# Kernel optimization log

Hardware: AMD Instinct MI355X
Metric: run time of the kernel (lower is better)

Reference implementation:

```python
import jax, jax.numpy as jnp
import numpy as np

B, T, H = 4, 2048, 512
HEADS = 8
D = H // HEADS  # head dim = 64


def setup_inputs() -> dict:
    key = jax.random.key(0)
    ks = jax.random.split(key, 5)
    s = 1.0 / np.sqrt(H)
    return {
        "x": jax.random.normal(ks[0], (B, T, H), dtype=jnp.float32),
        "w_qkv": jax.random.uniform(ks[1], (H, 3 * H), dtype=jnp.float32, minval=-s, maxval=s),
        "b_qkv": jax.random.uniform(ks[2], (3 * H,), dtype=jnp.float32, minval=-s, maxval=s),
        "w_proj": jax.random.uniform(ks[3], (H, H), dtype=jnp.float32, minval=-s, maxval=s),
        "b_proj": jax.random.uniform(ks[4], (H,), dtype=jnp.float32, minval=-s, maxval=s),
    }


def reference(x, w_qkv, b_qkv, w_proj, b_proj):
    b, t, h = x.shape
    scale = (h // HEADS) ** (-0.5)
    qkv = (x @ w_qkv + b_qkv).reshape(b, t, 3, HEADS, h // HEADS)
    q, k, v = qkv[:, :, 0], qkv[:, :, 1], qkv[:, :, 2]  # [b,t,heads,d]
    q = q * scale
    scores = jnp.einsum('bthd,bThd->bhtT', q, k)  # [b,heads,t,t]
    weights = jax.nn.softmax(scores, axis=-1)
    attn = jnp.einsum('bhtT,bThd->bthd', weights, v).reshape(b, t, h)
    return attn @ w_proj + b_proj
```

## Files before the change

kernel.cpp:

```cpp
#include <hip/hip_runtime.h>
#include <stdint.h>

typedef unsigned short u16;
typedef __attribute__((ext_vector_type(8))) __bf16 bf16x8;
typedef __attribute__((ext_vector_type(4))) __bf16 bf16x4;
typedef __attribute__((ext_vector_type(4))) float f32x4;
typedef __attribute__((ext_vector_type(2))) unsigned int u32x2;
typedef __attribute__((ext_vector_type(4))) unsigned int u32x4;

#define QSCALE 0.18033688011112042f

__device__ __forceinline__ u16 f2bf(float f) {
    uint32_t u = __builtin_bit_cast(uint32_t, f);
    u = (u + 0x7fffu + ((u >> 16) & 1u)) >> 16;
    return (u16)u;
}
__device__ __forceinline__ float bf2f(u16 h) {
    uint32_t u = ((uint32_t)h) << 16;
    return __builtin_bit_cast(float, u);
}

__device__ __forceinline__ void gl_lds16(const u16* g, u16* l) {
    __builtin_amdgcn_global_load_lds(
        (__attribute__((address_space(1))) uint32_t*)(g),
        (__attribute__((address_space(3))) uint32_t*)(l), 16, 0, 0);
}

__global__ __launch_bounds__(256) void convert_x_k(const float* __restrict__ xf,
                                                   u16* __restrict__ xbf) {
    const size_t v = (size_t)blockIdx.x * 256 + threadIdx.x;
    const f32x4 val = ((const f32x4*)xf)[v];
    u32x2 p;
    p.x = (uint32_t)f2bf(val.x) | ((uint32_t)f2bf(val.y) << 16);
    p.y = (uint32_t)f2bf(val.z) | ((uint32_t)f2bf(val.w) << 16);
    *(u32x2*)&xbf[v * 4] = p;
}

__global__ void transpose_cvt_k(const float* __restrict__ in,
                                u16* __restrict__ out, int R, int C) {
    __shared__ u16 t[64][65];
    const int bx = blockIdx.x << 6, by = blockIdx.y << 6;
    const int tx = threadIdx.x, ty = threadIdx.y;
#pragma unroll
    for (int i = ty; i < 64; i += 8)
        t[i][tx] = f2bf(in[(size_t)(by + i) * C + bx + tx]);
    __syncthreads();
#pragma unroll
    for (int i = ty; i < 64; i += 8) out[(size_t)(bx + i) * R + by + tx] = t[tx][i];
}

template <int EPI>
__global__ __launch_bounds__(256) void gemm_bt_k(
    const u16* __restrict__ A, const u16* __restrict__ Bt,
    const float* __restrict__ bias,
    u16* __restrict__ Qb, u16* __restrict__ Kb, u16* __restrict__ Vt,
    float* __restrict__ OutF) {
    __shared__ u16 lA[128 * 32];
    __shared__ u16 lB[128 * 32];
    const int tid = threadIdx.x;
    const int w = tid >> 6, l = tid & 63, quad = l >> 4, r = l & 15;
    const int tm = blockIdx.x << 7, tn = blockIdx.y << 7;
    const int wm = (w >> 1) << 6, wn = (w & 1) << 6;
    const int srow = l >> 2, sch = (l & 3) << 3;

    f32x4 acc[4][4];
#pragma unroll
    for (int i = 0; i < 4; ++i)
#pragma unroll
        for (int j = 0; j < 4; ++j) acc[i][j] = (f32x4){0.f, 0.f, 0.f, 0.f};

    for (int kk = 0; kk < 512; kk += 32) {
        __syncthreads();
#pragma unroll
        for (int ii = 0; ii < 2; ++ii) {
            const int rowl = w * 32 + ii * 16;
            gl_lds16(A + (size_t)(tm + rowl + srow) * 512 + kk + sch, &lA[rowl * 32]);
            gl_lds16(Bt + (size_t)(tn + rowl + srow) * 512 + kk + sch, &lB[rowl * 32]);
        }
        __syncthreads();
        bf16x8 af[4], bfr[4];
#pragma unroll
        for (int mi = 0; mi < 4; ++mi)
            af[mi] = *(const bf16x8*)&lA[(wm + mi * 16 + r) * 32 + quad * 8];
#pragma unroll
        for (int ni = 0; ni < 4; ++ni)
            bfr[ni] = *(const bf16x8*)&lB[(wn + ni * 16 + r) * 32 + quad * 8];
#pragma unroll
        for (int mi = 0; mi < 4; ++mi)
#pragma unroll
            for (int ni = 0; ni < 4; ++ni)
                acc[mi][ni] = __builtin_amdgcn_mfma_f32_16x16x32_bf16(
                    af[mi], bfr[ni], acc[mi][ni], 0, 0, 0);
    }

#pragma unroll
    for (int ni = 0; ni < 4; ++ni) {
        const int n = tn + wn + ni * 16 + r;
        const float bv = bias[n];
        const int which = n >> 9, head = (n >> 6) & 7, d = n & 63;
#pragma unroll
        for (int mi = 0; mi < 4; ++mi) {
#pragma unroll
            for (int i = 0; i < 4; ++i) {
                const int m = tm + wm + mi * 16 + quad * 4 + i;
                const float v = acc[mi][ni][i] + bv;
                if (EPI == 0) {
                    const int bb = m >> 11, t = m & 2047;
                    const int bh = bb * 8 + head;
                    if (which == 0)
                        Qb[((size_t)(bh * 2048 + t) << 6) + d] = f2bf(v * QSCALE);
                    else if (which == 1)
                        Kb[((size_t)(bh * 2048 + t) << 6) + d] = f2bf(v);
                    else
                        Vt[((size_t)(bh * 64 + d) << 11) + t] = f2bf(v);
                } else {
                    OutF[(size_t)m * 512 + n] = v;
                }
            }
        }
    }
}

__global__ __launch_bounds__(256) void attn_k(
    const u16* __restrict__ Qb, const u16* __restrict__ Kb,
    const u16* __restrict__ Vt, u16* __restrict__ attnb) {
    __shared__ u16 lk[64 * 64];
    __shared__ u16 lv[64 * 64];
    __shared__ u16 lp[4][16 * 72];
    const int tid = threadIdx.x;
    const int w = tid >> 6, l = tid & 63, quad = l >> 4, r = l & 15;
    const int qt = blockIdx.x, bh = blockIdx.y;
    const size_t qbase = (size_t)bh * 2048 + qt * 64;
    const int srl = l >> 3;
    const int sg = (l & 7) ^ srl;

    const bf16x8 qf0 = *(const bf16x8*)&Qb[((qbase + w * 16 + r) << 6) + quad * 8];
    const bf16x8 qf1 = *(const bf16x8*)&Qb[((qbase + w * 16 + r) << 6) + 32 + quad * 8];

    const int rl = r & 7;
    const int rhi = r >> 3;

    const u32x4 onesu = {0x3F803F80u, 0x3F803F80u, 0x3F803F80u, 0x3F803F80u};
    const bf16x8 vones = __builtin_bit_cast(bf16x8, onesu);

    f32x4 o[4];
#pragma unroll
    for (int i = 0; i < 4; ++i) o[i] = (f32x4){0.f, 0.f, 0.f, 0.f};
    f32x4 osum = (f32x4){0.f, 0.f, 0.f, 0.f};

    for (int kv0 = 0; kv0 < 2048; kv0 += 64) {
        __syncthreads();
#pragma unroll
        for (int ii = 0; ii < 2; ++ii) {
            const int chunk = w * 2 + ii;
            gl_lds16(Kb + ((size_t)(bh * 2048 + kv0 + chunk * 8 + srl) << 6) + sg * 8,
                     &lk[chunk * 512]);
            gl_lds16(Vt + (((size_t)(bh * 64 + chunk * 8 + srl)) << 11) + kv0 + sg * 8,
                     &lv[chunk * 512]);
        }
        __syncthreads();

#pragma unroll
        for (int kt = 0; kt < 4; ++kt) {
            const int base = (kt * 2 + rhi) * 512 + rl * 64;
            const bf16x8 a0 = *(const bf16x8*)&lk[base + (quad ^ rl) * 8];
            const bf16x8 a1 = *(const bf16x8*)&lk[base + ((quad ^ rl) ^ 4) * 8];
            f32x4 z = (f32x4){0.f, 0.f, 0.f, 0.f};
            z = __builtin_amdgcn_mfma_f32_16x16x32_bf16(a0, qf0, z, 0, 0, 0);
            z = __builtin_amdgcn_mfma_f32_16x16x32_bf16(a1, qf1, z, 0, 0, 0);
            const uint32_t u0 =
                __builtin_bit_cast(uint32_t, __builtin_amdgcn_exp2f(z[0])) + 0x8000u;
            const uint32_t u1 =
                __builtin_bit_cast(uint32_t, __builtin_amdgcn_exp2f(z[1])) + 0x8000u;
            const uint32_t u2 =
                __builtin_bit_cast(uint32_t, __builtin_amdgcn_exp2f(z[2])) + 0x8000u;
            const uint32_t u3 =
                __builtin_bit_cast(uint32_t, __builtin_amdgcn_exp2f(z[3])) + 0x8000u;
            const uint32_t lo = __builtin_amdgcn_perm(u1, u0, 0x07060302u);
            const uint32_t hi = __builtin_amdgcn_perm(u3, u2, 0x07060302u);
            const uint64_t both = (uint64_t)lo | ((uint64_t)hi << 32);
            *(bf16x4*)&lp[w][r * 72 + kt * 16 + quad * 4] =
                __builtin_bit_cast(bf16x4, both);
        }

        asm volatile("s_waitcnt lgkmcnt(0)" ::: "memory");

#pragma unroll
        for (int h = 0; h < 2; ++h) {
            const bf16x8 ap = *(const bf16x8*)&lp[w][r * 72 + h * 32 + quad * 8];
#pragma unroll
            for (int dt = 0; dt < 4; ++dt) {
                const int baseV = (dt * 2 + rhi) * 512 + rl * 64;
                const bf16x8 bv =
                    *(const bf16x8*)&lv[baseV + ((h * 4 + quad) ^ rl) * 8];
                o[dt] = __builtin_amdgcn_mfma_f32_16x16x32_bf16(ap, bv, o[dt], 0, 0, 0);
            }
            osum = __builtin_amdgcn_mfma_f32_16x16x32_bf16(ap, vones, osum, 0, 0, 0);
        }
    }

    const int bb = bh >> 3, head = bh & 7;
#pragma unroll
    for (int i = 0; i < 4; ++i) {
        const float inv = __builtin_amdgcn_rcpf(osum[i]);
        const int row = bb * 2048 + qt * 64 + w * 16 + quad * 4 + i;
#pragma unroll
        for (int dt = 0; dt < 4; ++dt)
            attnb[(size_t)row * 512 + head * 64 + dt * 16 + r] = f2bf(o[dt][i] * inv);
    }
}

extern "C" void kernel_launch(void* const* d_in, const int* in_sizes, int n_in,
                              void* d_out, int out_size, void* d_ws, size_t ws_size,
                              hipStream_t stream) {
    const float *x = nullptr, *wq = nullptr, *bq = nullptr, *wp = nullptr, *bp = nullptr;
    for (int i = 0; i < n_in; ++i) {
        switch (in_sizes[i]) {
            case 4194304: x  = (const float*)d_in[i]; break;
            case 786432:  wq = (const float*)d_in[i]; break;
            case 1536:    bq = (const float*)d_in[i]; break;
            case 262144:  wp = (const float*)d_in[i]; break;
            case 512:     bp = (const float*)d_in[i]; break;
        }
    }
    if (!x || !wq || !bq || !wp || !bp) {
        x = (const float*)d_in[0]; wq = (const float*)d_in[1];
        bq = (const float*)d_in[2]; wp = (const float*)d_in[3];
        bp = (const float*)d_in[4];
    }
    float* out = (float*)d_out;

    char* ws = (char*)d_ws;
    u16* attnb  = (u16*)(ws + 0);
    u16* wqkvT  = (u16*)(ws + 0);
    u16* Qb     = (u16*)(ws + 8388608);
    u16* wprojT = (u16*)(ws + 8388608);
    u16* Kb     = (u16*)(ws + 16777216);
    u16* Vt     = (u16*)(ws + 25165824);
    u16* xbf    = (u16*)d_out;

    convert_x_k<<<dim3(4096), 256, 0, stream>>>(x, xbf);
    transpose_cvt_k<<<dim3(24, 8), dim3(64, 8), 0, stream>>>(wq, wqkvT, 512, 1536);
    gemm_bt_k<0><<<dim3(64, 12), 256, 0, stream>>>(xbf, wqkvT, bq, Qb, Kb, Vt, nullptr);
    attn_k<<<dim3(32, 32), 256, 0, stream>>>(Qb, Kb, Vt, attnb);
    transpose_cvt_k<<<dim3(8, 8), dim3(64, 8), 0, stream>>>(wp, wprojT, 512, 512);
    gemm_bt_k<1><<<dim3(64, 4), 256, 0, stream>>>(attnb, wprojT, bp, nullptr, nullptr,
                                                  nullptr, out);
}
```

Before: 178.8 us.

## Double-buffer LDS tiles in GEMM and attention, add MFMA priority and P swizzle

Both the projection GEMM and the attention kernel now keep two LDS buffers. The next K/V (or A/B) tile is issued with global_load_lds while the current tile is computed, which also cuts the barriers per iteration from two to one. The attention kernel also raises wave priority around its MFMA sections with s_setprio. It replaces the padded P scratch (stride 72) with an XOR-swizzled unpadded layout to avoid LDS bank conflicts. The cost is twice the LDS for the K/V and A/B tiles, which may lower occupancy, and correctness relies on the end-of-loop barrier also waiting for the outstanding async loads.

```diff
diff --git a/kernel.cpp b/kernel.cpp
--- a/kernel.cpp
+++ b/kernel.cpp
@@ -55,8 +55,8 @@
     const float* __restrict__ bias,
     u16* __restrict__ Qb, u16* __restrict__ Kb, u16* __restrict__ Vt,
     float* __restrict__ OutF) {
-    __shared__ u16 lA[128 * 32];
-    __shared__ u16 lB[128 * 32];
+    __shared__ u16 lA[2][128 * 32];
+    __shared__ u16 lB[2][128 * 32];
     const int tid = threadIdx.x;
     const int w = tid >> 6, l = tid & 63, quad = l >> 4, r = l & 15;
     const int tm = blockIdx.x << 7, tn = blockIdx.y << 7;
@@ -69,28 +69,36 @@
 #pragma unroll
         for (int j = 0; j < 4; ++j) acc[i][j] = (f32x4){0.f, 0.f, 0.f, 0.f};
 
-    for (int kk = 0; kk < 512; kk += 32) {
-        __syncthreads();
+    auto stage = [&](int b, int kk) {
 #pragma unroll
         for (int ii = 0; ii < 2; ++ii) {
             const int rowl = w * 32 + ii * 16;
-            gl_lds16(A + (size_t)(tm + rowl + srow) * 512 + kk + sch, &lA[rowl * 32]);
-            gl_lds16(Bt + (size_t)(tn + rowl + srow) * 512 + kk + sch, &lB[rowl * 32]);
-        }
-        __syncthreads();
+            gl_lds16(A + (size_t)(tm + rowl + srow) * 512 + kk + sch, &lA[b][rowl * 32]);
+            gl_lds16(Bt + (size_t)(tn + rowl + srow) * 512 + kk + sch, &lB[b][rowl * 32]);
+        }
+    };
+
+    stage(0, 0);
+    __syncthreads();
+
+    int cur = 0;
+    for (int kk = 0; kk < 512; kk += 32) {
+        if (kk + 32 < 512) stage(cur ^ 1, kk + 32);
         bf16x8 af[4], bfr[4];
 #pragma unroll
         for (int mi = 0; mi < 4; ++mi)
-            af[mi] = *(const bf16x8*)&lA[(wm + mi * 16 + r) * 32 + quad * 8];
+            af[mi] = *(const bf16x8*)&lA[cur][(wm + mi * 16 + r) * 32 + quad * 8];
 #pragma unroll
         for (int ni = 0; ni < 4; ++ni)
-            bfr[ni] = *(const bf16x8*)&lB[(wn + ni * 16 + r) * 32 + quad * 8];
+            bfr[ni] = *(const bf16x8*)&lB[cur][(wn + ni * 16 + r) * 32 + quad * 8];
 #pragma unroll
         for (int mi = 0; mi < 4; ++mi)
 #pragma unroll
             for (int ni = 0; ni < 4; ++ni)
                 acc[mi][ni] = __builtin_amdgcn_mfma_f32_16x16x32_bf16(
                     af[mi], bfr[ni], acc[mi][ni], 0, 0, 0);
+        __syncthreads();
+        cur ^= 1;
     }
 
 #pragma unroll
@@ -124,9 +132,9 @@
 __global__ __launch_bounds__(256) void attn_k(
     const u16* __restrict__ Qb, const u16* __restrict__ Kb,
     const u16* __restrict__ Vt, u16* __restrict__ attnb) {
-    __shared__ u16 lk[64 * 64];
-    __shared__ u16 lv[64 * 64];
-    __shared__ u16 lp[4][16 * 72];
+    __shared__ u16 lk[2][64 * 64];
+    __shared__ u16 lv[2][64 * 64];
+    __shared__ u16 lp[4][16 * 64];
     const int tid = threadIdx.x;
     const int w = tid >> 6, l = tid & 63, quad = l >> 4, r = l & 15;
     const int qt = blockIdx.x, bh = blockIdx.y;
@@ -139,6 +147,7 @@
 
     const int rl = r & 7;
     const int rhi = r >> 3;
+    const int psw = rl << 3;
 
     const u32x4 onesu = {0x3F803F80u, 0x3F803F80u, 0x3F803F80u, 0x3F803F80u};
     const bf16x8 vones = __builtin_bit_cast(bf16x8, onesu);
@@ -148,26 +157,34 @@
     for (int i = 0; i < 4; ++i) o[i] = (f32x4){0.f, 0.f, 0.f, 0.f};
     f32x4 osum = (f32x4){0.f, 0.f, 0.f, 0.f};
 
-    for (int kv0 = 0; kv0 < 2048; kv0 += 64) {
-        __syncthreads();
+    auto stage = [&](int b, int kv0) {
 #pragma unroll
         for (int ii = 0; ii < 2; ++ii) {
             const int chunk = w * 2 + ii;
             gl_lds16(Kb + ((size_t)(bh * 2048 + kv0 + chunk * 8 + srl) << 6) + sg * 8,
-                     &lk[chunk * 512]);
+                     &lk[b][chunk * 512]);
             gl_lds16(Vt + (((size_t)(bh * 64 + chunk * 8 + srl)) << 11) + kv0 + sg * 8,
-                     &lv[chunk * 512]);
-        }
-        __syncthreads();
+                     &lv[b][chunk * 512]);
+        }
+    };
+
+    stage(0, 0);
+    __syncthreads();
+
+    int cur = 0;
+    for (int kv0 = 0; kv0 < 2048; kv0 += 64) {
+        if (kv0 + 64 < 2048) stage(cur ^ 1, kv0 + 64);
 
 #pragma unroll
         for (int kt = 0; kt < 4; ++kt) {
             const int base = (kt * 2 + rhi) * 512 + rl * 64;
-            const bf16x8 a0 = *(const bf16x8*)&lk[base + (quad ^ rl) * 8];
-            const bf16x8 a1 = *(const bf16x8*)&lk[base + ((quad ^ rl) ^ 4) * 8];
+            const bf16x8 a0 = *(const bf16x8*)&lk[cur][base + (quad ^ rl) * 8];
+            const bf16x8 a1 = *(const bf16x8*)&lk[cur][base + ((quad ^ rl) ^ 4) * 8];
             f32x4 z = (f32x4){0.f, 0.f, 0.f, 0.f};
+            __builtin_amdgcn_s_setprio(1);
             z = __builtin_amdgcn_mfma_f32_16x16x32_bf16(a0, qf0, z, 0, 0, 0);
             z = __builtin_amdgcn_mfma_f32_16x16x32_bf16(a1, qf1, z, 0, 0, 0);
+            __builtin_amdgcn_s_setprio(0);
             const uint32_t u0 =
                 __builtin_bit_cast(uint32_t, __builtin_amdgcn_exp2f(z[0])) + 0x8000u;
             const uint32_t u1 =
@@ -179,24 +196,30 @@
             const uint32_t lo = __builtin_amdgcn_perm(u1, u0, 0x07060302u);
             const uint32_t hi = __builtin_amdgcn_perm(u3, u2, 0x07060302u);
             const uint64_t both = (uint64_t)lo | ((uint64_t)hi << 32);
-            *(bf16x4*)&lp[w][r * 72 + kt * 16 + quad * 4] =
+            *(bf16x4*)&lp[w][r * 64 + ((kt * 16 + quad * 4) ^ psw)] =
                 __builtin_bit_cast(bf16x4, both);
         }
 
         asm volatile("s_waitcnt lgkmcnt(0)" ::: "memory");
 
+        __builtin_amdgcn_s_setprio(1);
 #pragma unroll
         for (int h = 0; h < 2; ++h) {
-            const bf16x8 ap = *(const bf16x8*)&lp[w][r * 72 + h * 32 + quad * 8];
+            const bf16x8 ap =
+                *(const bf16x8*)&lp[w][r * 64 + ((h * 32 + quad * 8) ^ psw)];
 #pragma unroll
             for (int dt = 0; dt < 4; ++dt) {
                 const int baseV = (dt * 2 + rhi) * 512 + rl * 64;
                 const bf16x8 bv =
-                    *(const bf16x8*)&lv[baseV + ((h * 4 + quad) ^ rl) * 8];
+                    *(const bf16x8*)&lv[cur][baseV + ((h * 4 + quad) ^ rl) * 8];
                 o[dt] = __builtin_amdgcn_mfma_f32_16x16x32_bf16(ap, bv, o[dt], 0, 0, 0);
             }
             osum = __builtin_amdgcn_mfma_f32_16x16x32_bf16(ap, vones, osum, 0, 0, 0);
         }
+        __builtin_amdgcn_s_setprio(0);
+
+        __syncthreads();
+        cur ^= 1;
     }
 
     const int bb = bh >> 3, head = bh & 7;
```

Result: no change. 175.8 us (-1.7%).
